# Kernel optimization log

Hardware: AMD Instinct MI355X
Metric: run time of the kernel (lower is better)

The kernel has to match this reference:

```python
import jax, jax.numpy as jnp
import numpy as np
import math

D_MODEL = 1024
N_HEADS = 16
D_K = 64
CHUNK_LEN = 64


def setup_inputs() -> dict:
    key = jax.random.key(0)
    ks = jax.random.split(key, 12)
    hd = N_HEADS * D_K
    s = 0.02
    return {
        'h': jax.random.normal(ks[0], (4, 2048, D_MODEL), jnp.float32),
        'e': jax.random.normal(ks[1], (4, 32, 2, 128, D_MODEL), jnp.float32),
        'Wq': jax.random.normal(ks[2], (D_MODEL, hd), jnp.float32) * s,
        'bq': jnp.zeros((hd,), jnp.float32),
        'Wk': jax.random.normal(ks[3], (D_MODEL, hd), jnp.float32) * s,
        'bk': jnp.zeros((hd,), jnp.float32),
        'Wv': jax.random.normal(ks[4], (D_MODEL, hd), jnp.float32) * s,
        'bv': jnp.zeros((hd,), jnp.float32),
        'Wo': jax.random.normal(ks[5], (hd, D_MODEL), jnp.float32) * s,
        'bo': jnp.zeros((D_MODEL,), jnp.float32),
        'gamma': jnp.ones((D_MODEL,), jnp.float32),
        'beta': jnp.zeros((D_MODEL,), jnp.float32),
    }


def reference(h, e, Wq, bq, Wk, bk, Wv, bv, Wo, bo, gamma, beta):
    b, chunks, neighbors, nlen, d_model = e.shape
    seq_len = h.shape[1]
    scale = 1.0 / math.sqrt(D_K)
    h_res = h
    # shift so chunk i attends to neighbors retrieved for chunk i
    hh = h[:, CHUNK_LEN - 1:]
    # layer norm
    mu = jnp.mean(hh, axis=-1, keepdims=True)
    var = jnp.mean(jnp.square(hh - mu), axis=-1, keepdims=True)
    hh = (hh - mu) / jnp.sqrt(var + 1e-5) * gamma + beta
    # pad to chunks * CHUNK_LEN
    pad = chunks * CHUNK_LEN - hh.shape[1]
    hh = jnp.pad(hh, ((0, 0), (0, pad), (0, 0)))
    hh = hh.reshape(b, chunks, CHUNK_LEN, d_model)
    q = (hh @ Wq + bq).reshape(b, chunks, CHUNK_LEN, N_HEADS, D_K)
    k = (e @ Wk + bk).reshape(b, chunks, neighbors, nlen, N_HEADS, D_K)
    v = (e @ Wv + bv).reshape(b, chunks, neighbors, nlen, N_HEADS, D_K)
    attn = jnp.einsum('bcihd,bcnjhd->bchinj', q, k) * scale  # [b,c,h,i,n,j]
    a_shape = attn.shape
    attn = jax.nn.softmax(attn.reshape(*a_shape[:-2], -1), axis=-1).reshape(a_shape)
    out = jnp.einsum('bchinj,bcnjhd->bcihd', attn, v)
    out = out.reshape(b, chunks * CHUNK_LEN, N_HEADS * D_K)
    out = out @ Wo + bo
    out = jnp.pad(out, ((0, 0), (CHUNK_LEN - 1, 0), (0, 0)))
    return out[:, :seq_len] + h_res
```

## Files before the change

kernel.cpp:

```cpp
#include <hip/hip_runtime.h>
#include <cstdint>
#include <cstddef>


typedef float f32x4 __attribute__((ext_vector_type(4)));
typedef __bf16 bf16x8 __attribute__((ext_vector_type(8)));

static __device__ __forceinline__ ushort f2bf(float f) {
  union { float f; uint32_t u; } x; x.f = f;
  uint32_t r = x.u + 0x7fffu + ((x.u >> 16) & 1u);
  return (ushort)(r >> 16);
}

static __device__ __forceinline__ bf16x8 ld_frag(const ushort* p) {
  union { uint4 u; bf16x8 v; } x;
  x.u = *(const uint4*)p;
  return x.v;
}

static __device__ __forceinline__ void gl2lds16(const ushort* g, ushort* l) {
  __builtin_amdgcn_global_load_lds(
      (const __attribute__((address_space(1))) void*)g,
      (__attribute__((address_space(3))) void*)l,
      16, 0, 0);
}

__global__ __launch_bounds__(256) void transpose_cast4(const float* __restrict__ Wq,
                                                       const float* __restrict__ Wk,
                                                       const float* __restrict__ Wv,
                                                       const float* __restrict__ Wo,
                                                       ushort* __restrict__ WqT,
                                                       ushort* __restrict__ WkvT,
                                                       ushort* __restrict__ WoT) {
  const float* W; ushort* WT;
  switch (blockIdx.z) {
    case 0:  W = Wq; WT = WqT; break;
    case 1:  W = Wk; WT = WkvT; break;
    case 2:  W = Wv; WT = WkvT + (size_t)1024 * 1024; break;
    default: W = Wo; WT = WoT; break;
  }
  __shared__ float tile[64][65];
  const int t = threadIdx.x;
  const int n0 = blockIdx.x * 64, k0 = blockIdx.y * 64;
#pragma unroll
  for (int i = 0; i < 4; ++i) {
    int lid = i * 256 + t;
    int r = lid >> 4, c4 = (lid & 15) * 4;
    float4 v = *(const float4*)&W[(size_t)(k0 + r) * 1024 + n0 + c4];
    tile[r][c4 + 0] = v.x; tile[r][c4 + 1] = v.y;
    tile[r][c4 + 2] = v.z; tile[r][c4 + 3] = v.w;
  }
  __syncthreads();
#pragma unroll
  for (int i = 0; i < 4; ++i) {
    int lid = i * 256 + t;
    int n = lid >> 4, k4 = (lid & 15) * 4;
    ushort4 o;
    o.x = f2bf(tile[k4 + 0][n]); o.y = f2bf(tile[k4 + 1][n]);
    o.z = f2bf(tile[k4 + 2][n]); o.w = f2bf(tile[k4 + 3][n]);
    *(ushort4*)&WT[(size_t)(n0 + n) * 1024 + k0 + k4] = o;
  }
}

__global__ __launch_bounds__(256) void cast_bf16(const float* __restrict__ x,
                                                 ushort* __restrict__ y) {
  const size_t i = ((size_t)blockIdx.x * 256 + threadIdx.x) * 8;
  float4 a = *(const float4*)&x[i];
  float4 b = *(const float4*)&x[i + 4];
  ushort o[8];
  o[0] = f2bf(a.x); o[1] = f2bf(a.y); o[2] = f2bf(a.z); o[3] = f2bf(a.w);
  o[4] = f2bf(b.x); o[5] = f2bf(b.y); o[6] = f2bf(b.z); o[7] = f2bf(b.w);
  *(uint4*)&y[i] = *(const uint4*)o;
}

__global__ __launch_bounds__(256) void ln_kernel(const float* __restrict__ h,
                                                 const float* __restrict__ gamma,
                                                 const float* __restrict__ beta,
                                                 ushort* __restrict__ hh) {
  const int bx = blockIdx.x;
  const int b = bx >> 11, s = bx & 2047;
  const int t = threadIdx.x;
  ushort* orow = hh + (size_t)(b * 2048 + s) * 1024;
  if (s >= 1985) {
    ushort4 z; z.x = 0; z.y = 0; z.z = 0; z.w = 0;
    *(ushort4*)&orow[t * 4] = z;
    return;
  }
  const float* xrow = h + (size_t)(b * 2048 + 63 + s) * 1024;
  float4 x = *(const float4*)&xrow[t * 4];
  float s1 = x.x + x.y + x.z + x.w;
  float s2 = x.x * x.x + x.y * x.y + x.z * x.z + x.w * x.w;
#pragma unroll
  for (int off = 32; off > 0; off >>= 1) {
    s1 += __shfl_xor(s1, off);
    s2 += __shfl_xor(s2, off);
  }
  __shared__ float a1[4], a2[4];
  if ((t & 63) == 0) { a1[t >> 6] = s1; a2[t >> 6] = s2; }
  __syncthreads();
  s1 = a1[0] + a1[1] + a1[2] + a1[3];
  s2 = a2[0] + a2[1] + a2[2] + a2[3];
  const float mu = s1 * (1.0f / 1024.0f);
  const float var = s2 * (1.0f / 1024.0f) - mu * mu;
  const float rstd = rsqrtf(var + 1e-5f);
  float4 g = *(const float4*)&gamma[t * 4];
  float4 be = *(const float4*)&beta[t * 4];
  ushort4 o;
  o.x = f2bf((x.x - mu) * rstd * g.x + be.x);
  o.y = f2bf((x.y - mu) * rstd * g.y + be.y);
  o.z = f2bf((x.z - mu) * rstd * g.z + be.z);
  o.w = f2bf((x.w - mu) * rstd * g.w + be.w);
  *(ushort4*)&orow[t * 4] = o;
}

template <int MODE, int NT>
__global__ __launch_bounds__(256) void gemm_bf16(const ushort* __restrict__ A,
                                                 const ushort* __restrict__ Bt,
                                                 const float* __restrict__ bias,
                                                 const float* __restrict__ bias2,
                                                 ushort* __restrict__ Cbf,
                                                 ushort* __restrict__ Vtg,
                                                 float* __restrict__ Cf,
                                                 const float* __restrict__ resid,
                                                 int mtiles, float scale,
                                                 int mrow_off) {
  if constexpr (MODE == 1) {
    if (blockIdx.x >= 512) {
      const int idx4 = (blockIdx.x - 512) * 256 + threadIdx.x;
      const int b = idx4 / 16128;
      const int rem = idx4 - b * 16128;
      const size_t o = (size_t)b * 2048 * 1024 + (size_t)rem * 4;
      *(float4*)&Cf[o] = *(const float4*)&resid[o];
      return;
    }
  }
  __shared__ __align__(16) ushort Alds[2][128 * 32];
  __shared__ __align__(16) ushort Blds[2][128 * 32];
  const int t = threadIdx.x;
  const int lane = t & 63, wave = t >> 6;
  const int quad = lane >> 4, l16 = lane & 15;

  const int L = blockIdx.x;
  const int xcd = L & 7, slot = L >> 3;
  const int nt = slot & (NT - 1);
  const int mt = xcd * (mtiles >> 3) + (slot / NT);
  const int m0 = mt * 128, n0 = nt * 128;

  const int srow = lane >> 2;
  const int scol = (lane & 3) * 8;
  const int c0 = wave * 2;
  const ushort* gA0 = A  + (size_t)(m0 + c0 * 16 + srow) * 1024 + scol;
  const ushort* gA1 = gA0 + 16 * 1024;
  const ushort* gB0 = Bt + (size_t)(n0 + c0 * 16 + srow) * 1024 + scol;
  const ushort* gB1 = gB0 + 16 * 1024;
  ushort* dA0 = &Alds[0][c0 * 512 + lane * 8];
  ushort* dA1 = dA0 + 512;
  ushort* dB0 = &Blds[0][c0 * 512 + lane * 8];
  ushort* dB1 = dB0 + 512;
  const ptrdiff_t SUB = 128 * 32;

  const int wrow = (wave >> 1) * 64, wcol = (wave & 1) * 64;
  const ushort* pA = &Alds[0][(wrow + l16) * 32 + quad * 8];
  const ushort* pB = &Blds[0][(wcol + l16) * 32 + quad * 8];

  f32x4 zero = {0.f, 0.f, 0.f, 0.f};
  f32x4 acc[4][4];
#pragma unroll
  for (int i = 0; i < 4; ++i)
#pragma unroll
    for (int j = 0; j < 4; ++j) acc[i][j] = zero;

  for (int kb = 0; kb < 16; ++kb) {
    const int ko = kb * 64;
    gl2lds16(gA0 + ko, dA0);         gl2lds16(gA1 + ko, dA1);
    gl2lds16(gA0 + ko + 32, dA0 + SUB); gl2lds16(gA1 + ko + 32, dA1 + SUB);
    gl2lds16(gB0 + ko, dB0);         gl2lds16(gB1 + ko, dB1);
    gl2lds16(gB0 + ko + 32, dB0 + SUB); gl2lds16(gB1 + ko + 32, dB1 + SUB);
    __syncthreads();
#pragma unroll
    for (int sub = 0; sub < 2; ++sub) {
      bf16x8 af[4], bfv[4];
#pragma unroll
      for (int i = 0; i < 4; ++i) af[i]  = ld_frag(pA + sub * SUB + i * 512);
#pragma unroll
      for (int j = 0; j < 4; ++j) bfv[j] = ld_frag(pB + sub * SUB + j * 512);
#pragma unroll
      for (int i = 0; i < 4; ++i)
#pragma unroll
        for (int j = 0; j < 4; ++j)
          acc[i][j] = __builtin_amdgcn_mfma_f32_16x16x32_bf16(af[i], bfv[j], acc[i][j], 0, 0, 0);
    }
    __syncthreads();
  }

#pragma unroll
  for (int mi = 0; mi < 4; ++mi)
#pragma unroll
    for (int mj = 0; mj < 4; ++mj) {
      const int cc = n0 + wcol + mj * 16 + l16;
      const int r0 = m0 + wrow + mi * 16 + quad * 4;
      if constexpr (MODE == 0) {
        const float bvb = bias[cc];
#pragma unroll
        for (int rr = 0; rr < 4; ++rr)
          Cbf[(size_t)(r0 + rr) * 1024 + cc] = f2bf((acc[mi][mj][rr] + bvb) * scale);
      } else {
        const float bvb = bias[cc];
#pragma unroll
        for (int rr = 0; rr < 4; ++rr) {
          const int r = r0 + rr;
          const int b = r >> 11, s = r & 2047;
          if (s < 1985) {
            const size_t o = (size_t)(b * 2048 + s + 63) * 1024 + cc;
            Cf[o] = acc[mi][mj][rr] + bvb + resid[o];
          }
        }
      }
    }
}

__global__ __launch_bounds__(512, 2) void gemm_kv256(const ushort* __restrict__ A,
                                                     const ushort* __restrict__ Bt,
                                                     const float* __restrict__ bk_,
                                                     const float* __restrict__ bv_,
                                                     ushort* __restrict__ Kout,
                                                     ushort* __restrict__ Vtg,
                                                     int mrow_off) {
  __shared__ __align__(16) ushort Alds[4 * 8192];
  __shared__ __align__(16) ushort Blds[4 * 8192];

  const int t = threadIdx.x;
  const int lane = t & 63, wave = t >> 6;
  const int wm = wave >> 2, wn = wave & 3;
  const int l16 = lane & 15, quad = lane >> 4;

  const int L = blockIdx.x;
  const int xcd = L & 7, slot = L >> 3;
  const int nt = slot & 7, mt = xcd * 8 + (slot >> 3);
  const int m0 = mt * 256, n0 = nt * 256;

  const int w2 = wave * 2;
  const int srow = lane >> 3;
  const int lanex = (lane & 7) ^ srow;
  const ushort* gA2 = A  + (size_t)(m0 + w2 * 8 + srow) * 1024 + lanex * 8;
  const ushort* gB2 = Bt + (size_t)(n0 + w2 * 8 + srow) * 1024 + lanex * 8;
  ushort* dA2 = Alds + w2 * 512 + lane * 8;
  ushort* dB2 = Blds + w2 * 512 + lane * 8;

  auto stage_a = [&](int ti, int hh) {
    const ushort* g = gA2 + (size_t)hh * 131072 + (size_t)ti * 64;
    ushort* d = dA2 + ((ti & 1) * 2 + hh) * 8192;
    gl2lds16(g, d);
    gl2lds16(g + 8192, d + 512);
  };
  auto stage_b = [&](int ti, int hh) {
    const ushort* g = gB2 + (size_t)hh * 131072 + (size_t)ti * 64;
    ushort* d = dB2 + ((ti & 1) * 2 + hh) * 8192;
    gl2lds16(g, d);
    gl2lds16(g + 8192, d + 512);
  };

  const int b2 = (l16 >> 2) & 1;
  const int qx = (quad ^ (l16 & 3)) << 3;
  const int kof0 = b2 << 5;
  const int kof1 = 32 - kof0;

  f32x4 zero = {0.f, 0.f, 0.f, 0.f};
  f32x4 acc[8][4];
#pragma unroll
  for (int i = 0; i < 8; ++i)
#pragma unroll
    for (int j = 0; j < 4; ++j) acc[i][j] = zero;

  stage_b(0, 0); stage_a(0, 0); stage_b(0, 1); stage_a(0, 1);
  stage_b(1, 0); stage_a(1, 0); stage_b(1, 1);
  asm volatile("s_waitcnt vmcnt(6)" ::: "memory");
  __builtin_amdgcn_s_barrier();

  bf16x8 a[4][2], b01[2][2], b23[2][2];

#pragma unroll 2
  for (int tt = 0; tt < 16; ++tt) {
    const int cur = tt & 1;
    const ushort* pa = Alds + (cur * 2 + wm) * 8192 + l16 * 64 + qx;
    const ushort* pb = Blds + (cur * 2 + (wn >> 1)) * 8192 +
                       ((wn & 1) * 64 + l16) * 64 + qx;

#pragma unroll
    for (int mi = 0; mi < 4; ++mi) {
      a[mi][0] = ld_frag(pa + mi * 1024 + kof0);
      a[mi][1] = ld_frag(pa + mi * 1024 + kof1);
    }
#pragma unroll
    for (int ni = 0; ni < 2; ++ni) {
      b01[ni][0] = ld_frag(pb + ni * 1024 + kof0);
      b01[ni][1] = ld_frag(pb + ni * 1024 + kof1);
    }
    if (tt < 15) stage_a(tt + 1, 1);
    __builtin_amdgcn_s_barrier();
    asm volatile("s_waitcnt lgkmcnt(0)" ::: "memory");
    __builtin_amdgcn_sched_barrier(0);
    __builtin_amdgcn_s_setprio(1);
#pragma unroll
    for (int mi = 0; mi < 4; ++mi)
#pragma unroll
      for (int ni = 0; ni < 2; ++ni) {
        acc[mi][ni] = __builtin_amdgcn_mfma_f32_16x16x32_bf16(a[mi][0], b01[ni][0], acc[mi][ni], 0, 0, 0);
        acc[mi][ni] = __builtin_amdgcn_mfma_f32_16x16x32_bf16(a[mi][1], b01[ni][1], acc[mi][ni], 0, 0, 0);
      }
    __builtin_amdgcn_s_setprio(0);
    __builtin_amdgcn_s_barrier();

#pragma unroll
    for (int ni = 0; ni < 2; ++ni) {
      b23[ni][0] = ld_frag(pb + (ni + 2) * 1024 + kof0);
      b23[ni][1] = ld_frag(pb + (ni + 2) * 1024 + kof1);
    }
    if (tt < 14) stage_b(tt + 2, 0);
    __builtin_amdgcn_s_barrier();
    asm volatile("s_waitcnt lgkmcnt(0)" ::: "memory");
    __builtin_amdgcn_sched_barrier(0);
    __builtin_amdgcn_s_setprio(1);
#pragma unroll
    for (int mi = 0; mi < 4; ++mi)
#pragma unroll
      for (int ni = 0; ni < 2; ++ni) {
        acc[mi][ni + 2] = __builtin_amdgcn_mfma_f32_16x16x32_bf16(a[mi][0], b23[ni][0], acc[mi][ni + 2], 0, 0, 0);
        acc[mi][ni + 2] = __builtin_amdgcn_mfma_f32_16x16x32_bf16(a[mi][1], b23[ni][1], acc[mi][ni + 2], 0, 0, 0);
      }
    __builtin_amdgcn_s_setprio(0);
    __builtin_amdgcn_s_barrier();

#pragma unroll
    for (int mi = 0; mi < 4; ++mi) {
      a[mi][0] = ld_frag(pa + (mi + 4) * 1024 + kof0);
      a[mi][1] = ld_frag(pa + (mi + 4) * 1024 + kof1);
    }
    if (tt < 14) stage_b(tt + 2, 1);
    __builtin_amdgcn_s_barrier();
    asm volatile("s_waitcnt lgkmcnt(0)" ::: "memory");
    __builtin_amdgcn_sched_barrier(0);
    __builtin_amdgcn_s_setprio(1);
#pragma unroll
    for (int mi = 0; mi < 4; ++mi)
#pragma unroll
      for (int ni = 0; ni < 2; ++ni) {
        acc[mi + 4][ni + 2] = __builtin_amdgcn_mfma_f32_16x16x32_bf16(a[mi][0], b23[ni][0], acc[mi + 4][ni + 2], 0, 0, 0);
        acc[mi + 4][ni + 2] = __builtin_amdgcn_mfma_f32_16x16x32_bf16(a[mi][1], b23[ni][1], acc[mi + 4][ni + 2], 0, 0, 0);
      }
    __builtin_amdgcn_s_setprio(0);
    __builtin_amdgcn_s_barrier();

    if (tt < 14) stage_a(tt + 2, 0);
    __builtin_amdgcn_s_barrier();
    __builtin_amdgcn_s_setprio(1);
#pragma unroll
    for (int mi = 0; mi < 4; ++mi)
#pragma unroll
      for (int ni = 0; ni < 2; ++ni) {
        acc[mi + 4][ni] = __builtin_amdgcn_mfma_f32_16x16x32_bf16(a[mi][0], b01[ni][0], acc[mi + 4][ni], 0, 0, 0);
        acc[mi + 4][ni] = __builtin_amdgcn_mfma_f32_16x16x32_bf16(a[mi][1], b01[ni][1], acc[mi + 4][ni], 0, 0, 0);
      }
    __builtin_amdgcn_s_setprio(0);
    if (tt < 15) {
      if (tt == 14) asm volatile("s_waitcnt vmcnt(0)" ::: "memory");
      else          asm volatile("s_waitcnt vmcnt(6)" ::: "memory");
      __builtin_amdgcn_s_barrier();
    }
  }

  const int rbase = m0 + wm * 128 + quad * 4;
  const int cbase = n0 + wn * 64 + l16;
  if (n0 < 1024) {
#pragma unroll
    for (int mi = 0; mi < 8; ++mi)
#pragma unroll
      for (int ni = 0; ni < 4; ++ni) {
        const int cc = cbase + ni * 16;
        const float bb = bk_[cc];
        const int r0 = rbase + mi * 16;
#pragma unroll
        for (int rr = 0; rr < 4; ++rr)
          Kout[(size_t)(r0 + rr) * 1024 + cc] = f2bf(acc[mi][ni][rr] + bb);
      }
  } else {
#pragma unroll
    for (int mi = 0; mi < 8; ++mi)
#pragma unroll
      for (int ni = 0; ni < 4; ++ni) {
        const int cv = cbase - 1024 + ni * 16;
        const int hh_ = cv >> 6, dd = cv & 63;
        const float bb = bv_[cv];
        const int gr0 = rbase + mi * 16 + mrow_off;
        const int bcl = gr0 >> 8, j0 = gr0 & 255;
        ushort4 o;
        o.x = f2bf(acc[mi][ni][0] + bb);
        o.y = f2bf(acc[mi][ni][1] + bb);
        o.z = f2bf(acc[mi][ni][2] + bb);
        o.w = f2bf(acc[mi][ni][3] + bb);
        *(ushort4*)&Vtg[(size_t)(bcl * 16 + hh_) * 16384 + dd * 256 + j0] = o;
      }
  }
}

__global__ __launch_bounds__(256) void attn_kernel(const ushort* __restrict__ Qb,
                                                   const ushort* __restrict__ Kb,
                                                   const ushort* __restrict__ Vtg,
                                                   ushort* __restrict__ Ob) {
  __shared__ __align__(16) ushort smem[4608 + 18432 + 16896];
  __shared__ float redm[4][64];
  __shared__ float reds[4][64];
  ushort* Qs = smem;
  ushort* Ks = smem + 4608;
  ushort* Vt = smem + 23040;
  ushort* Ps = smem;

  const int t = threadIdx.x;
  const int bx = blockIdx.x;
  const int hd = bx & 15, c = (bx >> 4) & 31, b = bx >> 9;
  const int lane = t & 63, wave = t >> 6;
  const int quad = lane >> 4, l16 = lane & 15;

  const int qrow0 = b * 2048 + c * 64;
  const int kvrow0 = (b * 32 + c) * 256;
  const int colh = hd * 64;
  const ushort* vsrc = Vtg + ((size_t)((b * 32 + c) * 16 + hd)) * 16384;

  uint4 qreg[2], kreg[8], vreg[8];
#pragma unroll
  for (int it = 0; it < 2; ++it) {
    int lid = it * 256 + t;
    qreg[it] = *(const uint4*)&Qb[(size_t)(qrow0 + (lid >> 3)) * 1024 + colh + (lid & 7) * 8];
  }
#pragma unroll
  for (int it = 0; it < 8; ++it) {
    int lid = it * 256 + t;
    kreg[it] = *(const uint4*)&Kb[(size_t)(kvrow0 + (lid >> 3)) * 1024 + colh + (lid & 7) * 8];
  }
#pragma unroll
  for (int it = 0; it < 8; ++it) {
    int lid = it * 256 + t;
    vreg[it] = *(const uint4*)&vsrc[(lid >> 5) * 256 + (lid & 31) * 8];
  }
#pragma unroll
  for (int it = 0; it < 2; ++it) {
    int lid = it * 256 + t;
    *(uint4*)&Qs[(lid >> 3) * 72 + (lid & 7) * 8] = qreg[it];
  }
#pragma unroll
  for (int it = 0; it < 8; ++it) {
    int lid = it * 256 + t;
    *(uint4*)&Ks[(lid >> 3) * 72 + (lid & 7) * 8] = kreg[it];
  }
  __syncthreads();

  const int jw = wave * 64;
  f32x4 zero = {0.f, 0.f, 0.f, 0.f};
  f32x4 acc[4][4];
#pragma unroll
  for (int i = 0; i < 4; ++i)
#pragma unroll
    for (int j = 0; j < 4; ++j) acc[i][j] = zero;

  __builtin_amdgcn_s_setprio(1);
#pragma unroll
  for (int kb = 0; kb < 2; ++kb) {
    bf16x8 af[4], bfv[4];
#pragma unroll
    for (int mi = 0; mi < 4; ++mi)
      af[mi] = ld_frag(&Qs[(mi * 16 + l16) * 72 + kb * 32 + quad * 8]);
#pragma unroll
    for (int mj = 0; mj < 4; ++mj)
      bfv[mj] = ld_frag(&Ks[(jw + mj * 16 + l16) * 72 + kb * 32 + quad * 8]);
#pragma unroll
    for (int mi = 0; mi < 4; ++mi)
#pragma unroll
      for (int mj = 0; mj < 4; ++mj)
        acc[mi][mj] = __builtin_amdgcn_mfma_f32_16x16x32_bf16(af[mi], bfv[mj], acc[mi][mj], 0, 0, 0);
  }
  __builtin_amdgcn_s_setprio(0);

#pragma unroll
  for (int it = 0; it < 8; ++it) {
    int lid = it * 256 + t;
    *(uint4*)&Vt[(lid >> 5) * 264 + (lid & 31) * 8] = vreg[it];
  }

  float rmax[4][4];
#pragma unroll
  for (int mi = 0; mi < 4; ++mi)
#pragma unroll
    for (int rr = 0; rr < 4; ++rr) {
      float m = fmaxf(fmaxf(acc[mi][0][rr], acc[mi][1][rr]),
                      fmaxf(acc[mi][2][rr], acc[mi][3][rr]));
      m = fmaxf(m, __shfl_xor(m, 1));
      m = fmaxf(m, __shfl_xor(m, 2));
      m = fmaxf(m, __shfl_xor(m, 4));
      m = fmaxf(m, __shfl_xor(m, 8));
      rmax[mi][rr] = m;
    }
  if (l16 == 0) {
#pragma unroll
    for (int mi = 0; mi < 4; ++mi)
#pragma unroll
      for (int rr = 0; rr < 4; ++rr)
        redm[wave][mi * 16 + quad * 4 + rr] = rmax[mi][rr];
  }
  __syncthreads();
  float gmax[4][4];
#pragma unroll
  for (int mi = 0; mi < 4; ++mi)
#pragma unroll
    for (int rr = 0; rr < 4; ++rr) {
      const int row = mi * 16 + quad * 4 + rr;
      gmax[mi][rr] = fmaxf(fmaxf(redm[0][row], redm[1][row]),
                           fmaxf(redm[2][row], redm[3][row]));
    }
  float rsum[4][4];
#pragma unroll
  for (int mi = 0; mi < 4; ++mi)
#pragma unroll
    for (int rr = 0; rr < 4; ++rr) {
      float s = 0.f;
#pragma unroll
      for (int mj = 0; mj < 4; ++mj) {
        float p = exp2f((acc[mi][mj][rr] - gmax[mi][rr]) * 1.4426950408889634f);
        acc[mi][mj][rr] = p;
        s += p;
      }
      s += __shfl_xor(s, 1);
      s += __shfl_xor(s, 2);
      s += __shfl_xor(s, 4);
      s += __shfl_xor(s, 8);
      rsum[mi][rr] = s;
    }
  if (l16 == 0) {
#pragma unroll
    for (int mi = 0; mi < 4; ++mi)
#pragma unroll
      for (int rr = 0; rr < 4; ++rr)
        reds[wave][mi * 16 + quad * 4 + rr] = rsum[mi][rr];
  }
  __syncthreads();
#pragma unroll
  for (int mi = 0; mi < 4; ++mi)
#pragma unroll
    for (int rr = 0; rr < 4; ++rr) {
      const int row = mi * 16 + quad * 4 + rr;
      const float inv = 1.0f / (reds[0][row] + reds[1][row] + reds[2][row] + reds[3][row]);
#pragma unroll
      for (int mj = 0; mj < 4; ++mj)
        Ps[row * 264 + jw + mj * 16 + l16] = f2bf(acc[mi][mj][rr] * inv);
    }
  __syncthreads();

  const int d0 = wave * 16;
  f32x4 acc2[4];
#pragma unroll
  for (int mi = 0; mi < 4; ++mi) acc2[mi] = zero;
  __builtin_amdgcn_s_setprio(1);
#pragma unroll
  for (int kb = 0; kb < 8; ++kb) {
    bf16x8 bfv = ld_frag(&Vt[(d0 + l16) * 264 + kb * 32 + quad * 8]);
#pragma unroll
    for (int mi = 0; mi < 4; ++mi) {
      bf16x8 af = ld_frag(&Ps[(mi * 16 + l16) * 264 + kb * 32 + quad * 8]);
      acc2[mi] = __builtin_amdgcn_mfma_f32_16x16x32_bf16(af, bfv, acc2[mi], 0, 0, 0);
    }
  }
  __builtin_amdgcn_s_setprio(0);
#pragma unroll
  for (int mi = 0; mi < 4; ++mi)
#pragma unroll
    for (int rr = 0; rr < 4; ++rr) {
      const int i = mi * 16 + quad * 4 + rr;
      Ob[(size_t)(qrow0 + i) * 1024 + colh + d0 + l16] = f2bf(acc2[mi][rr]);
    }
}

extern "C" void kernel_launch(void* const* d_in, const int* in_sizes, int n_in,
                              void* d_out, int out_size, void* d_ws, size_t ws_size,
                              hipStream_t stream) {
  const float* h     = (const float*)d_in[0];
  const float* e     = (const float*)d_in[1];
  const float* Wq    = (const float*)d_in[2];
  const float* bq    = (const float*)d_in[3];
  const float* Wk    = (const float*)d_in[4];
  const float* bk    = (const float*)d_in[5];
  const float* Wv    = (const float*)d_in[6];
  const float* bv    = (const float*)d_in[7];
  const float* Wo    = (const float*)d_in[8];
  const float* bo    = (const float*)d_in[9];
  const float* gamma = (const float*)d_in[10];
  const float* beta  = (const float*)d_in[11];
  float* out = (float*)d_out;

  char* ws = (char*)d_ws;
  ushort* stg  = (ushort*)(ws + ((size_t)0 << 20));
  ushort* WqT  = (ushort*)(ws + ((size_t)32 << 20));
  ushort* WkvT = (ushort*)(ws + ((size_t)34 << 20));
  ushort* WoT  = (ushort*)(ws + ((size_t)38 << 20));
  ushort* Qb   = (ushort*)(ws + ((size_t)40 << 20));
  ushort* Kb   = (ushort*)(ws + ((size_t)56 << 20));
  ushort* VtG  = (ushort*)(ws + ((size_t)120 << 20));

  transpose_cast4<<<dim3(16, 16, 4), 256, 0, stream>>>(Wq, Wk, Wv, Wo, WqT, WkvT, WoT);

  ln_kernel<<<8192, 256, 0, stream>>>(h, gamma, beta, stg);

  gemm_bf16<0, 8><<<512, 256, 0, stream>>>(stg, WqT, bq, nullptr, Qb, nullptr,
                                           nullptr, nullptr, 64, 0.125f, 0);

  for (int half = 0; half < 2; ++half) {
    const size_t roff = (size_t)half * 16384 * 1024;
    cast_bf16<<<8192, 256, 0, stream>>>(e + roff, stg);
    gemm_kv256<<<512, 512, 0, stream>>>(stg, WkvT, bk, bv, Kb + roff,
                                        VtG, half * 16384);
  }

  attn_kernel<<<2048, 256, 0, stream>>>(Qb, Kb, VtG, stg);

  gemm_bf16<1, 8><<<764, 256, 0, stream>>>(stg, WoT, bo, nullptr, nullptr, nullptr,
                                           out, h, 64, 1.0f, 0);
}
```

Measured before the change: 528.6 us.

## Load K and V MFMA fragments directly from global into registers, shrink LDS

```diff
diff --git a/kernel.cpp b/kernel.cpp
--- a/kernel.cpp
+++ b/kernel.cpp
@@ -15,6 +15,12 @@
 static __device__ __forceinline__ bf16x8 ld_frag(const ushort* p) {
   union { uint4 u; bf16x8 v; } x;
   x.u = *(const uint4*)p;
+  return x.v;
+}
+
+static __device__ __forceinline__ bf16x8 u4_frag(uint4 u) {
+  union { uint4 u; bf16x8 v; } x;
+  x.u = u;
   return x.v;
 }
 
@@ -403,17 +409,14 @@
   }
 }
 
-__global__ __launch_bounds__(256) void attn_kernel(const ushort* __restrict__ Qb,
-                                                   const ushort* __restrict__ Kb,
-                                                   const ushort* __restrict__ Vtg,
-                                                   ushort* __restrict__ Ob) {
-  __shared__ __align__(16) ushort smem[4608 + 18432 + 16896];
+__global__ __launch_bounds__(256, 3) void attn_kernel(const ushort* __restrict__ Qb,
+                                                      const ushort* __restrict__ Kb,
+                                                      const ushort* __restrict__ Vtg,
+                                                      ushort* __restrict__ Ob) {
+  __shared__ __align__(16) ushort Qs[64 * 72];
+  __shared__ __align__(16) ushort Ps[64 * 264];
   __shared__ float redm[4][64];
   __shared__ float reds[4][64];
-  ushort* Qs = smem;
-  ushort* Ks = smem + 4608;
-  ushort* Vt = smem + 23040;
-  ushort* Ps = smem;
 
   const int t = threadIdx.x;
   const int bx = blockIdx.x;
@@ -426,35 +429,23 @@
   const int colh = hd * 64;
   const ushort* vsrc = Vtg + ((size_t)((b * 32 + c) * 16 + hd)) * 16384;
 
-  uint4 qreg[2], kreg[8], vreg[8];
+  const int jw = wave * 64;
+  bf16x8 kf[4][2];
+#pragma unroll
+  for (int mj = 0; mj < 4; ++mj)
+#pragma unroll
+    for (int kb = 0; kb < 2; ++kb)
+      kf[mj][kb] = ld_frag(&Kb[(size_t)(kvrow0 + jw + mj * 16 + l16) * 1024 +
+                               colh + kb * 32 + quad * 8]);
+
 #pragma unroll
   for (int it = 0; it < 2; ++it) {
     int lid = it * 256 + t;
-    qreg[it] = *(const uint4*)&Qb[(size_t)(qrow0 + (lid >> 3)) * 1024 + colh + (lid & 7) * 8];
-  }
-#pragma unroll
-  for (int it = 0; it < 8; ++it) {
-    int lid = it * 256 + t;
-    kreg[it] = *(const uint4*)&Kb[(size_t)(kvrow0 + (lid >> 3)) * 1024 + colh + (lid & 7) * 8];
-  }
-#pragma unroll
-  for (int it = 0; it < 8; ++it) {
-    int lid = it * 256 + t;
-    vreg[it] = *(const uint4*)&vsrc[(lid >> 5) * 256 + (lid & 31) * 8];
-  }
-#pragma unroll
-  for (int it = 0; it < 2; ++it) {
-    int lid = it * 256 + t;
-    *(uint4*)&Qs[(lid >> 3) * 72 + (lid & 7) * 8] = qreg[it];
-  }
-#pragma unroll
-  for (int it = 0; it < 8; ++it) {
-    int lid = it * 256 + t;
-    *(uint4*)&Ks[(lid >> 3) * 72 + (lid & 7) * 8] = kreg[it];
+    uint4 v = *(const uint4*)&Qb[(size_t)(qrow0 + (lid >> 3)) * 1024 + colh + (lid & 7) * 8];
+    *(uint4*)&Qs[(lid >> 3) * 72 + (lid & 7) * 8] = v;
   }
   __syncthreads();
 
-  const int jw = wave * 64;
   f32x4 zero = {0.f, 0.f, 0.f, 0.f};
   f32x4 acc[4][4];
 #pragma unroll
@@ -465,26 +456,23 @@
   __builtin_amdgcn_s_setprio(1);
 #pragma unroll
   for (int kb = 0; kb < 2; ++kb) {
-    bf16x8 af[4], bfv[4];
+    bf16x8 af[4];
 #pragma unroll
     for (int mi = 0; mi < 4; ++mi)
       af[mi] = ld_frag(&Qs[(mi * 16 + l16) * 72 + kb * 32 + quad * 8]);
 #pragma unroll
-    for (int mj = 0; mj < 4; ++mj)
-      bfv[mj] = ld_frag(&Ks[(jw + mj * 16 + l16) * 72 + kb * 32 + quad * 8]);
-#pragma unroll
     for (int mi = 0; mi < 4; ++mi)
 #pragma unroll
       for (int mj = 0; mj < 4; ++mj)
-        acc[mi][mj] = __builtin_amdgcn_mfma_f32_16x16x32_bf16(af[mi], bfv[mj], acc[mi][mj], 0, 0, 0);
+        acc[mi][mj] = __builtin_amdgcn_mfma_f32_16x16x32_bf16(af[mi], kf[mj][kb], acc[mi][mj], 0, 0, 0);
   }
   __builtin_amdgcn_s_setprio(0);
 
-#pragma unroll
-  for (int it = 0; it < 8; ++it) {
-    int lid = it * 256 + t;
-    *(uint4*)&Vt[(lid >> 5) * 264 + (lid & 31) * 8] = vreg[it];
-  }
+  const int d0 = wave * 16;
+  bf16x8 vf[8];
+#pragma unroll
+  for (int kb = 0; kb < 8; ++kb)
+    vf[kb] = ld_frag(&vsrc[(d0 + l16) * 256 + kb * 32 + quad * 8]);
 
   float rmax[4][4];
 #pragma unroll
@@ -554,18 +542,16 @@
     }
   __syncthreads();
 
-  const int d0 = wave * 16;
   f32x4 acc2[4];
 #pragma unroll
   for (int mi = 0; mi < 4; ++mi) acc2[mi] = zero;
   __builtin_amdgcn_s_setprio(1);
 #pragma unroll
   for (int kb = 0; kb < 8; ++kb) {
-    bf16x8 bfv = ld_frag(&Vt[(d0 + l16) * 264 + kb * 32 + quad * 8]);
 #pragma unroll
     for (int mi = 0; mi < 4; ++mi) {
       bf16x8 af = ld_frag(&Ps[(mi * 16 + l16) * 264 + kb * 32 + quad * 8]);
-      acc2[mi] = __builtin_amdgcn_mfma_f32_16x16x32_bf16(af, bfv, acc2[mi], 0, 0, 0);
+      acc2[mi] = __builtin_amdgcn_mfma_f32_16x16x32_bf16(af, vf[kb], acc2[mi], 0, 0, 0);
     }
   }
   __builtin_amdgcn_s_setprio(0);
```

After: 503.9 us. 4.7% less time.
